# Kernel optimization log

Hardware: AMD Instinct MI355X
Metric: run time of the kernel (lower is better)

The kernel has to match this reference:

```python
import jax, jax.numpy as jnp
import numpy as np

B, L, D = 4, 2048, 1024
H, DK, DV, CS = 4, 128, 256, 16  # heads, head_qk_dim, head_v_dim, chunk_size
KD, VD = H * DK, H * DV          # 512, 1024
CONV = 4
EPS = 1e-5


def silu(x):
    return x * jax.nn.sigmoid(x)


def setup_inputs():
    key = jax.random.key(0)
    ks = jax.random.split(key, 9)
    s = 0.02
    return {
        "hidden_states": jax.random.normal(ks[0], (B, L, D), jnp.float32),
        "conv_w": jax.random.normal(ks[1], (D, CONV), jnp.float32) * 0.2,
        "Wq": jax.random.normal(ks[2], (KD, D), jnp.float32) * s,
        "Wk": jax.random.normal(ks[3], (KD, D), jnp.float32) * s,
        "Wv": jax.random.normal(ks[4], (VD, D), jnp.float32) * s,
        "Wb": jax.random.normal(ks[5], (H, D), jnp.float32) * s,
        "Wg": jax.random.normal(ks[6], (VD, D), jnp.float32) * s,
        "Wo": jax.random.normal(ks[7], (D, VD), jnp.float32) * s,
        "norm_w": jnp.ones((DV,), jnp.float32),
    }


def short_conv(x, w):
    # causal depthwise conv1d with SiLU activation: x [B,L,D], w [D,K]
    K = w.shape[1]
    xp = jnp.pad(x, ((0, 0), (K - 1, 0), (0, 0)))
    y = sum(xp[:, j:j + x.shape[1], :] * w[:, j] for j in range(K))
    return silu(y)


def delta_rule_chunk(q, k, v, beta):
    # fused_chunk_delta_rule: q,k [B,H,L,DK], v [B,H,L,DV], beta [B,H,L]
    b, h, l, dk = q.shape
    dv = v.shape[-1]
    nc = l // CS
    k = k * jax.lax.rsqrt(jnp.sum(k * k, -1, keepdims=True) + 1e-12)  # L2-normalize keys
    q = q * (dk ** -0.5)
    qc = q.reshape(b, h, nc, CS, dk)
    kc = k.reshape(b, h, nc, CS, dk)
    vc = v.reshape(b, h, nc, CS, dv)
    bc = beta.reshape(b, h, nc, CS)
    kb = kc * bc[..., None]
    # WY representation: T = (I + strict_tril(diag(beta) K K^T))^{-1}
    A = jnp.einsum('bhncd,bhnmd->bhncm', kb, kc)
    strict = jnp.tril(jnp.ones((CS, CS), q.dtype), -1)
    M = jnp.eye(CS, dtype=q.dtype) + A * strict
    eye = jnp.broadcast_to(jnp.eye(CS, dtype=q.dtype), M.shape)
    T = jax.scipy.linalg.solve_triangular(M, eye, lower=True)
    w = jnp.einsum('bhncm,bhnmd->bhncd', T, kb)
    u = jnp.einsum('bhncm,bhnmd->bhncd', T, vc * bc[..., None])
    causal = jnp.tril(jnp.ones((CS, CS), q.dtype))

    def step(S, inp):
        qi, ki, wi, ui = inp  # [B,H,CS,dk/dv]
        u_adj = ui - jnp.einsum('bhcd,bhdv->bhcv', wi, S)
        attn = jnp.einsum('bhcd,bhmd->bhcm', qi, ki) * causal
        o = jnp.einsum('bhcd,bhdv->bhcv', qi, S) + jnp.einsum('bhcm,bhmv->bhcv', attn, u_adj)
        S = S + jnp.einsum('bhcd,bhcv->bhdv', ki, u_adj)
        return S, o

    xs = tuple(jnp.moveaxis(t, 2, 0) for t in (qc, kc, w, u))
    S0 = jnp.zeros((b, h, dk, dv), q.dtype)
    _, os_ = jax.lax.scan(step, S0, xs)
    return jnp.moveaxis(os_, 0, 2).reshape(b, h, l, dv)


def reference(hidden_states, conv_w, Wq, Wk, Wv, Wb, Wg, Wo, norm_w):
    x = short_conv(hidden_states, conv_w)
    q = (x @ Wq.T).reshape(B, L, H, DK).transpose(0, 2, 1, 3)
    k = (x @ Wk.T).reshape(B, L, H, DK).transpose(0, 2, 1, 3)
    v = (x @ Wv.T).reshape(B, L, H, DV).transpose(0, 2, 1, 3)
    beta = jax.nn.sigmoid(x @ Wb.T).transpose(0, 2, 1)  # [B,H,L]
    o = delta_rule_chunk(q, k, v, beta)                 # [B,H,L,DV]
    o = o.transpose(0, 2, 1, 3)                          # [B,L,H,DV]
    g = (x @ Wg.T).reshape(B, L, H, DV)
    o = o * jax.lax.rsqrt(jnp.mean(o * o, -1, keepdims=True) + EPS) * norm_w * silu(g)
    return o.reshape(B, L, VD) @ Wo.T
```

## Files before the change

### kernel.cpp

```cpp
#include <hip/hip_runtime.h>
#include <cstdint>
#include <cstddef>

typedef _Float16 f16;
typedef _Float16 f16x4 __attribute__((ext_vector_type(4)));
typedef _Float16 f16x8 __attribute__((ext_vector_type(8)));
typedef float floatx4 __attribute__((ext_vector_type(4)));

#define MFMA32(a,b,c) __builtin_amdgcn_mfma_f32_16x16x32_f16((a),(b),(c),0,0,0)

#define ROWS 8192
#define NCHUNK 128
static constexpr float QSCALE = 0.08838834764831845f;

static __device__ __forceinline__ float sigmoidf_(float x) { return 1.0f / (1.0f + expf(-x)); }

static __device__ __forceinline__ uint32_t pack2(f16 a, f16 b) {
  union { f16 h[2]; uint32_t u; } v; v.h[0] = a; v.h[1] = b; return v.u;
}

#define GLOAD_LDS(gptr, lptr)                                                  \
  __builtin_amdgcn_global_load_lds(                                            \
      (const __attribute__((address_space(1))) void*)(gptr),                   \
      (__attribute__((address_space(3))) void*)(lptr), 16, 0, 0)

#define WAITV(N) do { asm volatile("s_waitcnt vmcnt(" #N ")" ::: "memory");    \
                      __builtin_amdgcn_sched_barrier(0); } while (0)

__global__ __launch_bounds__(256) void wconv_kernel(
    const float* __restrict__ Wq, const float* __restrict__ Wk,
    const float* __restrict__ Wv, const float* __restrict__ Wg,
    const float* __restrict__ Wo,
    f16* __restrict__ WcatHi, f16* __restrict__ WcatLoKV, f16* __restrict__ WoHi) {
  int tid = blockIdx.x * 256 + threadIdx.x;
  int e8 = tid * 8;
  if (e8 < 3145728) {
    int row = e8 >> 10, col = e8 & 1023;
    const float* src;
    if (row < 512)       src = Wk + (size_t)row * 1024 + col;
    else if (row < 1536) src = Wv + (size_t)(row - 512) * 1024 + col;
    else if (row < 2048) src = Wq + (size_t)(row - 1536) * 1024 + col;
    else                 src = Wg + (size_t)(row - 2048) * 1024 + col;
    f16 thi[8] __attribute__((aligned(16)));
    f16 tlo[8] __attribute__((aligned(16)));
#pragma unroll
    for (int j = 0; j < 8; j++) {
      float x = src[j];
      f16 h = (f16)x;
      thi[j] = h;
      tlo[j] = (f16)(x - (float)h);
    }
    *(uint4*)&WcatHi[e8] = *(const uint4*)thi;
    if (row < 1536) *(uint4*)&WcatLoKV[e8] = *(const uint4*)tlo;
  } else {
    int idx = e8 - 3145728;
    f16 t[8] __attribute__((aligned(16)));
#pragma unroll
    for (int j = 0; j < 8; j++) t[j] = (f16)Wo[idx + j];
    *(uint4*)&WoHi[idx] = *(const uint4*)t;
  }
}

__global__ __launch_bounds__(256) void conv_kernel(
    const float* __restrict__ hs, const float* __restrict__ cw,
    f16* __restrict__ xhi, f16* __restrict__ xlo) {
  int row = blockIdx.x;
  int b = row >> 11, l = row & 2047;
  int d = threadIdx.x * 4;
  floatx4 w0 = *(const floatx4*)&cw[(d + 0) * 4];
  floatx4 w1 = *(const floatx4*)&cw[(d + 1) * 4];
  floatx4 w2 = *(const floatx4*)&cw[(d + 2) * 4];
  floatx4 w3 = *(const floatx4*)&cw[(d + 3) * 4];
  floatx4 acc = {0.f, 0.f, 0.f, 0.f};
#pragma unroll
  for (int j = 0; j < 4; j++) {
    int ls = l - 3 + j;
    if (ls < 0) continue;
    floatx4 hv = *(const floatx4*)&hs[(size_t)(b * 2048 + ls) * 1024 + d];
    acc[0] += hv[0] * w0[j];
    acc[1] += hv[1] * w1[j];
    acc[2] += hv[2] * w2[j];
    acc[3] += hv[3] * w3[j];
  }
  f16 ohi[4] __attribute__((aligned(8)));
  f16 olo[4] __attribute__((aligned(8)));
#pragma unroll
  for (int q = 0; q < 4; q++) {
    float y = acc[q] * sigmoidf_(acc[q]);
    f16 h = (f16)y;
    ohi[q] = h;
    olo[q] = (f16)(y - (float)h);
  }
  *(uint2*)&xhi[(size_t)row * 1024 + d] = *(const uint2*)ohi;
  *(uint2*)&xlo[(size_t)row * 1024 + d] = *(const uint2*)olo;
}

__global__ __launch_bounds__(256) void beta_kernel(
    const f16* __restrict__ xhi, const f16* __restrict__ xlo,
    const float* __restrict__ Wb, float* __restrict__ betaf) {
  int row = blockIdx.x;
  int t = threadIdx.x;
  __shared__ floatx4 red[256];
  int c = t * 4;
  float xv[4];
#pragma unroll
  for (int j = 0; j < 4; j++)
    xv[j] = (float)xhi[(size_t)row * 1024 + c + j] + (float)xlo[(size_t)row * 1024 + c + j];
  floatx4 p = {0.f, 0.f, 0.f, 0.f};
#pragma unroll
  for (int hh = 0; hh < 4; hh++) {
    const float* wr = Wb + hh * 1024 + c;
    p[hh] = xv[0] * wr[0] + xv[1] * wr[1] + xv[2] * wr[2] + xv[3] * wr[3];
  }
  red[t] = p;
  __syncthreads();
  for (int s = 128; s > 0; s >>= 1) {
    if (t < s) red[t] += red[t + s];
    __syncthreads();
  }
  if (t < 4) betaf[(size_t)row * 4 + t] = sigmoidf_(red[0][t]);
}

__global__ __launch_bounds__(256) void gemm_hilo_kv(
    const f16* __restrict__ Ahi, const f16* __restrict__ Alo,
    const f16* __restrict__ Bhi, const f16* __restrict__ Blo,
    f16* __restrict__ ChHi, f16* __restrict__ ChLo, int K) {
  __shared__ __attribute__((aligned(16))) f16 AsH[128][40];
  __shared__ __attribute__((aligned(16))) f16 AsL[128][40];
  __shared__ __attribute__((aligned(16))) f16 BsH[128][40];
  __shared__ __attribute__((aligned(16))) f16 BsL[128][40];
  const int t = threadIdx.x;
  const int lane = t & 63, wave = t >> 6;
  const int lc = lane & 15, quad = lane >> 4;
  const int wm = (wave >> 1) * 64, wn = (wave & 1) * 64;
  const int m0 = blockIdx.y * 128, n0 = blockIdx.x * 128;
  const int r = t >> 2, c8 = (t & 3) * 8;
  floatx4 acc[4][4] = {};
  for (int kt = 0; kt < K; kt += 32) {
    __syncthreads();
    *(uint4*)&AsH[r][c8]      = *(const uint4*)&Ahi[(size_t)(m0 + r) * K + kt + c8];
    *(uint4*)&AsH[r + 64][c8] = *(const uint4*)&Ahi[(size_t)(m0 + r + 64) * K + kt + c8];
    *(uint4*)&AsL[r][c8]      = *(const uint4*)&Alo[(size_t)(m0 + r) * K + kt + c8];
    *(uint4*)&AsL[r + 64][c8] = *(const uint4*)&Alo[(size_t)(m0 + r + 64) * K + kt + c8];
    *(uint4*)&BsH[r][c8]      = *(const uint4*)&Bhi[(size_t)(n0 + r) * K + kt + c8];
    *(uint4*)&BsH[r + 64][c8] = *(const uint4*)&Bhi[(size_t)(n0 + r + 64) * K + kt + c8];
    *(uint4*)&BsL[r][c8]      = *(const uint4*)&Blo[(size_t)(n0 + r) * K + kt + c8];
    *(uint4*)&BsL[r + 64][c8] = *(const uint4*)&Blo[(size_t)(n0 + r + 64) * K + kt + c8];
    __syncthreads();
    f16x8 ah[4], al[4], bh2[4], bl[4];
#pragma unroll
    for (int i = 0; i < 4; i++) {
      ah[i] = *(const f16x8*)&AsH[wm + i * 16 + lc][quad * 8];
      al[i] = *(const f16x8*)&AsL[wm + i * 16 + lc][quad * 8];
    }
#pragma unroll
    for (int j = 0; j < 4; j++) {
      bh2[j] = *(const f16x8*)&BsH[wn + j * 16 + lc][quad * 8];
      bl[j]  = *(const f16x8*)&BsL[wn + j * 16 + lc][quad * 8];
    }
#pragma unroll
    for (int i = 0; i < 4; i++)
#pragma unroll
      for (int j = 0; j < 4; j++) {
        acc[i][j] = MFMA32(ah[i], bh2[j], acc[i][j]);
        acc[i][j] = MFMA32(al[i], bh2[j], acc[i][j]);
        acc[i][j] = MFMA32(ah[i], bl[j], acc[i][j]);
      }
  }
#pragma unroll
  for (int i = 0; i < 4; i++)
#pragma unroll
    for (int j = 0; j < 4; j++)
#pragma unroll
      for (int rr = 0; rr < 4; rr++) {
        int row = m0 + wm + i * 16 + quad * 4 + rr;
        int col = n0 + wn + j * 16 + lc;
        float x = acc[i][j][rr];
        f16 h = (f16)x;
        ChHi[(size_t)row * 3072 + col] = h;
        ChLo[(size_t)row * 1536 + col] = (f16)(x - (float)h);
      }
}

template <int OUTF16>
__global__ __launch_bounds__(256) void gemm_plain(
    const f16* __restrict__ A, const f16* __restrict__ Bw,
    f16* __restrict__ Ch, float* __restrict__ Cf, int K, int ldc) {
  __shared__ __attribute__((aligned(16))) f16 As[128][40];
  __shared__ __attribute__((aligned(16))) f16 Bs[128][40];
  const int t = threadIdx.x;
  const int lane = t & 63, wave = t >> 6;
  const int lc = lane & 15, quad = lane >> 4;
  const int wm = (wave >> 1) * 64, wn = (wave & 1) * 64;
  const int m0 = blockIdx.y * 128, n0 = blockIdx.x * 128;
  const int r = t >> 2, c8 = (t & 3) * 8;
  floatx4 acc[4][4] = {};
  for (int kt = 0; kt < K; kt += 32) {
    __syncthreads();
    *(uint4*)&As[r][c8]      = *(const uint4*)&A[(size_t)(m0 + r) * K + kt + c8];
    *(uint4*)&As[r + 64][c8] = *(const uint4*)&A[(size_t)(m0 + r + 64) * K + kt + c8];
    *(uint4*)&Bs[r][c8]      = *(const uint4*)&Bw[(size_t)(n0 + r) * K + kt + c8];
    *(uint4*)&Bs[r + 64][c8] = *(const uint4*)&Bw[(size_t)(n0 + r + 64) * K + kt + c8];
    __syncthreads();
    f16x8 af[4], bf[4];
#pragma unroll
    for (int i = 0; i < 4; i++) af[i] = *(const f16x8*)&As[wm + i * 16 + lc][quad * 8];
#pragma unroll
    for (int j = 0; j < 4; j++) bf[j] = *(const f16x8*)&Bs[wn + j * 16 + lc][quad * 8];
#pragma unroll
    for (int i = 0; i < 4; i++)
#pragma unroll
      for (int j = 0; j < 4; j++) acc[i][j] = MFMA32(af[i], bf[j], acc[i][j]);
  }
#pragma unroll
  for (int i = 0; i < 4; i++)
#pragma unroll
    for (int j = 0; j < 4; j++)
#pragma unroll
      for (int rr = 0; rr < 4; rr++) {
        int row = m0 + wm + i * 16 + quad * 4 + rr;
        int col = n0 + wn + j * 16 + lc;
        if (OUTF16) Ch[(size_t)row * ldc + col] = (f16)acc[i][j][rr];
        else        Cf[(size_t)row * ldc + col] = acc[i][j][rr];
      }
}

__global__ __launch_bounds__(256) void prepass_kernel(
    const f16* __restrict__ qkvgHi, const f16* __restrict__ kvLo,
    const float* __restrict__ betaf,
    f16* __restrict__ wHi, f16* __restrict__ wLo,
    f16* __restrict__ kTHi, f16* __restrict__ kTLo,
    f16* __restrict__ uHi, f16* __restrict__ uLo,
    float* __restrict__ attno) {
  int bid = blockIdx.x;
  int bh = bid >> 7, n = bid & 127;
  int b = bh >> 2, h = bh & 3;
  int t = threadIdx.x;

  __shared__ __attribute__((aligned(16))) float kc[16][132];
  __shared__ __attribute__((aligned(16))) float qc[16][132];
  __shared__ __attribute__((aligned(16))) float vb[16][260];
  __shared__ float Mm[16][16];
  __shared__ float Tt[16][16];
  __shared__ float Tb[16][16];
  __shared__ float part[16][16];
  __shared__ float betas[16];
  __shared__ float nrm[16];

  const size_t rowbase = (size_t)(b * 2048 + n * 16);
  {
    int i = t >> 4, o8 = (t & 15) * 8;
    size_t oh = (rowbase + i) * 3072;
    size_t ol = (rowbase + i) * 1536;
#pragma unroll
    for (int j = 0; j < 8; j++)
      kc[i][o8 + j] = (float)qkvgHi[oh + h * 128 + o8 + j] +
                      (float)kvLo[ol + h * 128 + o8 + j];
#pragma unroll
    for (int j = 0; j < 8; j++)
      qc[i][o8 + j] = (float)qkvgHi[oh + 1536 + h * 128 + o8 + j];
  }
  if (t < 16) betas[t] = betaf[(rowbase + t) * 4 + h];
  __syncthreads();
  {
    int i = t >> 4, sg = t & 15;
    float s = 0.f;
#pragma unroll
    for (int j = 0; j < 8; j++) { float v = kc[i][sg * 8 + j]; s += v * v; }
    part[i][sg] = s;
  }
  __syncthreads();
  if (t < 16) {
    float s = 0.f;
#pragma unroll
    for (int j = 0; j < 16; j++) s += part[t][j];
    nrm[t] = rsqrtf(s + 1e-12f);
  }
  __syncthreads();
  {
    int i = t >> 4, o8 = (t & 15) * 8;
    float sc = nrm[i];
#pragma unroll
    for (int j = 0; j < 8; j++) kc[i][o8 + j] *= sc;
  }
  __syncthreads();
  {
    int d = t & 127, ih = t >> 7;
    f16 thi[8] __attribute__((aligned(16)));
    f16 tlo[8] __attribute__((aligned(16)));
#pragma unroll
    for (int j = 0; j < 8; j++) {
      float x = kc[ih * 8 + j][d];
      f16 hh = (f16)x;
      thi[j] = hh;
      tlo[j] = (f16)(x - (float)hh);
    }
    size_t base = ((size_t)bh * 128 + n) * 2048 + d * 16 + ih * 8;
    *(uint4*)&kTHi[base] = *(const uint4*)thi;
    *(uint4*)&kTLo[base] = *(const uint4*)tlo;
  }
  {
    int i = t >> 4, j = t & 15;
    float s = 0.f;
    for (int x = 0; x < 128; x += 4)
      s += kc[i][x] * kc[j][x] + kc[i][x + 1] * kc[j][x + 1] +
           kc[i][x + 2] * kc[j][x + 2] + kc[i][x + 3] * kc[j][x + 3];
    Mm[i][j] = (i == j ? 1.f : 0.f) + ((j < i) ? betas[i] * s : 0.f);
  }
  __syncthreads();
  if (t < 16) {
    int j = t;
    float Tc[16];
#pragma unroll
    for (int i = 0; i < 16; i++) Tc[i] = 0.f;
    Tc[j] = 1.f;
    for (int i = j + 1; i < 16; i++) {
      float s = 0.f;
      for (int k2 = j; k2 < i; k2++) s += Mm[i][k2] * Tc[k2];
      Tc[i] = -s;
    }
    for (int i = 0; i < 16; i++) Tt[i][j] = Tc[i];
  }
  __syncthreads();
  { int i = t >> 4, m = t & 15; Tb[i][m] = Tt[i][m] * betas[m]; }
  {
    int m = t >> 4, c16 = (t & 15) * 16;
    size_t oh = (rowbase + m) * 3072 + 512 + h * 256 + c16;
    size_t ol = (rowbase + m) * 1536 + 512 + h * 256 + c16;
    float bm = betas[m];
#pragma unroll
    for (int j = 0; j < 16; j++)
      vb[m][c16 + j] = bm * ((float)qkvgHi[oh + j] + (float)kvLo[ol + j]);
  }
  __syncthreads();
  {
    int i = t >> 4, dg = t & 15;
    f16 thi[8] __attribute__((aligned(16)));
    f16 tlo[8] __attribute__((aligned(16)));
#pragma unroll
    for (int dd = 0; dd < 8; dd++) {
      int d = dg * 8 + dd;
      float s = 0.f;
#pragma unroll
      for (int m = 0; m < 16; m++) s += Tb[i][m] * kc[m][d];
      s = -s;
      f16 hh = (f16)s;
      thi[dd] = hh;
      tlo[dd] = (f16)(s - (float)hh);
    }
    size_t base = ((size_t)bh * 128 + n) * 2048 + i * 128 + dg * 8;
    *(uint4*)&wHi[base] = *(const uint4*)thi;
    *(uint4*)&wLo[base] = *(const uint4*)tlo;
  }
  {
    int v = t;
    f16 thi[16] __attribute__((aligned(16)));
    f16 tlo[16] __attribute__((aligned(16)));
#pragma unroll
    for (int i = 0; i < 16; i++) {
      float s2 = 0.f;
#pragma unroll
      for (int m = 0; m < 16; m++) s2 += Tt[i][m] * vb[m][v];
      f16 hh = (f16)s2;
      thi[i] = hh;
      tlo[i] = (f16)(s2 - (float)hh);
    }
    size_t base = ((((size_t)(v >> 4) * 16 + bh) * 128 + n) * 16 + (v & 15)) * 16;
    ((uint4*)&uHi[base])[0] = ((const uint4*)thi)[0];
    ((uint4*)&uHi[base])[1] = ((const uint4*)thi)[1];
    ((uint4*)&uLo[base])[0] = ((const uint4*)tlo)[0];
    ((uint4*)&uLo[base])[1] = ((const uint4*)tlo)[1];
  }
  {
    int i = t >> 4, j = t & 15;
    float s = 0.f;
    for (int x = 0; x < 128; x++) s += qc[i][x] * kc[j][x];
    attno[((size_t)bh * 128 + n) * 256 + i * 16 + j] = (j <= i) ? QSCALE * s : 0.f;
  }
}

#define STG_W   0
#define STG_WL  2048
#define STG_Q   4096
#define STG_KH  6144
#define STG_KL  8192
#define STG_SZ  10240

__global__ __launch_bounds__(64, 1) void scan_kernel(
    const f16* __restrict__ qkvgHi,
    const f16* __restrict__ wHi, const f16* __restrict__ wLo,
    const f16* __restrict__ kTHi, const f16* __restrict__ kTLo,
    const float* __restrict__ attn,
    const f16* __restrict__ uHi, const f16* __restrict__ uLo,
    float* __restrict__ o1, float* __restrict__ o2) {
  const int bid = blockIdx.x;
  const int slc = bid & 15, bh = bid >> 4;
  const int b = bh >> 2, h = bh & 3;
  const int v0 = slc * 16;
  const int lane = threadIdx.x;
  const int lc = lane & 15, quad = lane >> 4;
  const int qh = quad & 1;

  __shared__ __attribute__((aligned(16))) f16 stg[2][STG_SZ];
  __shared__ __attribute__((aligned(16))) f16 S_hi[16][136];
  __shared__ __attribute__((aligned(16))) f16 S_lo[16][136];

  floatx4 accS[8] = {};

  const size_t cb = (size_t)bh * 128;
  const f16* qb = qkvgHi + (size_t)b * 2048 * 3072 + 1536 + h * 128;
  const f16* ub  = uHi + ((size_t)(slc * 16 + bh)) * 0;
  (void)ub;
  const f16* ubH = uHi + ((size_t)(slc * 16 + bh)) * 128 * 256 + lc * 16 + quad * 4;
  const f16* ubL = uLo + ((size_t)(slc * 16 + bh)) * 128 * 256 + lc * 16 + quad * 4;
  const float* ab = attn + cb * 256 + lc * 16 + qh * 8;
  float* ob = (bh < 12) ? (o1 + (size_t)bh * 2048 * 256)
                        : (o2 + (size_t)(bh - 12) * 2048 * 256);

  int woff[4], koff[4], qoff[4];
#pragma unroll
  for (int p = 0; p < 4; p++) {
    int cid = p * 64 + lane;
    int row = cid >> 4, dgs = (cid & 15) ^ (row & 7);
    int d = cid >> 1,  ih = (cid & 1) ^ ((cid >> 3) & 1);
    woff[p] = row * 128 + dgs * 8;
    koff[p] = d * 16 + ih * 8;
    qoff[p] = row * 3072 + dgs * 8;
  }

  uint4 pa0[2], pa1[2];
  uint2 puh[2], pul[2];

  auto ISSUE_REG = [&](int slot, int nn) {
    pa0[slot] = *(const uint4*)(ab + (size_t)nn * 256);
    pa1[slot] = *(const uint4*)(ab + (size_t)nn * 256 + 4);
    puh[slot] = *(const uint2*)(ubH + (size_t)nn * 256);
    pul[slot] = *(const uint2*)(ubL + (size_t)nn * 256);
  };
  auto ISSUE_WQ = [&](int buf, int nn) {
    const f16* wsrc  = wHi + (cb + (size_t)nn) * 2048;
    const f16* wlsrc = wLo + (cb + (size_t)nn) * 2048;
    const f16* qsrc  = qb + (size_t)nn * 16 * 3072;
    f16* sbp = &stg[buf][0];
#pragma unroll
    for (int p = 0; p < 4; p++) {
      GLOAD_LDS(wsrc + woff[p],  sbp + STG_W  + p * 512);
      GLOAD_LDS(wlsrc + woff[p], sbp + STG_WL + p * 512);
      GLOAD_LDS(qsrc + qoff[p],  sbp + STG_Q  + p * 512);
    }
  };
  auto ISSUE_K = [&](int buf, int nn) {
    const f16* khsrc = kTHi + (cb + (size_t)nn) * 2048;
    const f16* klsrc = kTLo + (cb + (size_t)nn) * 2048;
    f16* sbp = &stg[buf][0];
#pragma unroll
    for (int p = 0; p < 4; p++) {
      GLOAD_LDS(khsrc + koff[p], sbp + STG_KH + p * 512);
      GLOAD_LDS(klsrc + koff[p], sbp + STG_KL + p * 512);
    }
  };

  ISSUE_REG(0, 0); ISSUE_WQ(0, 0); ISSUE_K(0, 0);
  ISSUE_REG(1, 1); ISSUE_WQ(1, 1); ISSUE_K(1, 1);

  for (int n = 0; n < NCHUNK; n += 2) {
#pragma unroll
    for (int hf = 0; hf < 2; hf++) {
      const int nn = n + hf;
      f16* sb = &stg[hf][0];

#pragma unroll
      for (int dt = 0; dt < 8; dt++) {
        f16x4 h4, l4;
#pragma unroll
        for (int r = 0; r < 4; r++) {
          float x = accS[dt][r];
          f16 hh = (f16)x;
          h4[r] = hh;
          l4[r] = (f16)(x - (float)hh);
        }
        *(f16x4*)&S_hi[lc][dt * 16 + quad * 4] = h4;
        *(f16x4*)&S_lo[lc][dt * 16 + quad * 4] = l4;
      }

      if (nn == 0)       WAITV(24);
      else if (nn < 127) WAITV(28);
      else               WAITV(4);

      floatx4 acc_u;
      {
        union { uint2 u2; f16 hh[4]; } Uh, Ul;
        Uh.u2 = puh[hf]; Ul.u2 = pul[hf];
#pragma unroll
        for (int r = 0; r < 4; r++) acc_u[r] = (float)Uh.hh[r] + (float)Ul.hh[r];
      }
      f16x8 aah, aal;
      {
        union { uint4 u4[2]; float f[8]; } PA;
        PA.u4[0] = pa0[hf]; PA.u4[1] = pa1[hf];
#pragma unroll
        for (int j = 0; j < 8; j++) {
          float a = PA.f[j];
          f16 ahh = (f16)a;
          aah[j] = ahh;
          aal[j] = (f16)(a - (float)ahh);
        }
      }
      if (nn + 2 < NCHUNK) ISSUE_REG(hf, nn + 2);

      f16x8 shf[4], slf[4], wah[4], wal[4], qah[4];
#pragma unroll
      for (int ks = 0; ks < 4; ks++) {
        shf[ks] = *(const f16x8*)&S_hi[lc][ks * 32 + quad * 8];
        slf[ks] = *(const f16x8*)&S_lo[lc][ks * 32 + quad * 8];
        int gi = lc * 128 + (((ks * 4 + quad) ^ (lc & 7)) * 8);
        wah[ks] = *(const f16x8*)(sb + STG_W  + gi);
        wal[ks] = *(const f16x8*)(sb + STG_WL + gi);
        qah[ks] = *(const f16x8*)(sb + STG_Q  + gi);
      }
      __builtin_amdgcn_sched_barrier(0);
      if (nn + 2 < NCHUNK) ISSUE_WQ(hf, nn + 2);

      floatx4 a1 = {0.f, 0.f, 0.f, 0.f}, a2 = {0.f, 0.f, 0.f, 0.f};
#pragma unroll
      for (int ks = 0; ks < 4; ks++) {
        acc_u = MFMA32(wah[ks], shf[ks], acc_u);
        a1    = MFMA32(wah[ks], slf[ks], a1);
        a2    = MFMA32(wal[ks], shf[ks], a2);
      }
      acc_u = acc_u + a1 + a2;
      floatx4 acc_o = {0.f, 0.f, 0.f, 0.f};
#pragma unroll
      for (int ks = 0; ks < 4; ks++) acc_o = MFMA32(qah[ks], shf[ks], acc_o);
#pragma unroll
      for (int ks = 0; ks < 4; ks++) acc_o = MFMA32(qah[ks], slf[ks], acc_o);

      f16x8 ubf;
      {
        f16 h0 = (f16)acc_u[0], h1 = (f16)acc_u[1];
        f16 h2 = (f16)acc_u[2], h3 = (f16)acc_u[3];
        uint32_t uh01 = pack2(h0, h1), uh23 = pack2(h2, h3);
        uint32_t ul01 = pack2((f16)(acc_u[0] - (float)h0), (f16)(acc_u[1] - (float)h1));
        uint32_t ul23 = pack2((f16)(acc_u[2] - (float)h2), (f16)(acc_u[3] - (float)h3));
        int srcA = (2 * qh) * 16 + lc;
        int srcB = srcA + 16;
        uint32_t Ah0 = __shfl((int)uh01, srcA, 64), Ah1 = __shfl((int)uh23, srcA, 64);
        uint32_t Bh0 = __shfl((int)uh01, srcB, 64), Bh1 = __shfl((int)uh23, srcB, 64);
        uint32_t Al0 = __shfl((int)ul01, srcA, 64), Al1 = __shfl((int)ul23, srcA, 64);
        uint32_t Bl0 = __shfl((int)ul01, srcB, 64), Bl1 = __shfl((int)ul23, srcB, 64);
        union { uint32_t u[4]; f16x8 v; } U;
        bool hi = (quad < 2);
        U.u[0] = hi ? Ah0 : Al0;
        U.u[1] = hi ? Ah1 : Al1;
        U.u[2] = hi ? Bh0 : Bl0;
        U.u[3] = hi ? Bh1 : Bl1;
        ubf = U.v;
      }
#pragma unroll
      for (int r = 0; r < 4; r++) acc_o[r] *= QSCALE;
      acc_o = MFMA32(aah, ubf, acc_o);
      acc_o = MFMA32(aal, ubf, acc_o);
#pragma unroll
      for (int r = 0; r < 4; r++)
        ob[(size_t)(nn * 16 + quad * 4 + r) * 256 + v0 + lc] = acc_o[r];

      const int kswz = (qh ^ ((lc >> 2) & 1)) * 8 + lc * 16;
#pragma unroll
      for (int dt = 0; dt < 8; dt++) {
        f16x8 kah = *(const f16x8*)(sb + STG_KH + dt * 256 + kswz);
        f16x8 kal = *(const f16x8*)(sb + STG_KL + dt * 256 + kswz);
        accS[dt] = MFMA32(kah, ubf, accS[dt]);
        accS[dt] = MFMA32(kal, ubf, accS[dt]);
      }
      __builtin_amdgcn_sched_barrier(0);
      if (nn + 2 < NCHUNK) ISSUE_K(hf, nn + 2);
    }
  }
}

__global__ __launch_bounds__(256) void gate_kernel(
    const float* __restrict__ o1, const float* __restrict__ o2,
    const f16* __restrict__ qkvgHi, const float* __restrict__ norm_w,
    f16* __restrict__ onh) {
  int h = threadIdx.x >> 6, lane = threadIdx.x & 63;
  int r = blockIdx.x;
  int b = r >> 11, l = r & 2047;
  int bh = b * 4 + h;
  const float* orow = ((bh < 12) ? (o1 + (size_t)bh * 524288)
                                 : (o2 + (size_t)(bh - 12) * 524288)) + (size_t)l * 256;
  int v = lane * 4;
  floatx4 ov = *(const floatx4*)&orow[v];
  float ss = ov[0] * ov[0] + ov[1] * ov[1] + ov[2] * ov[2] + ov[3] * ov[3];
  for (int m = 32; m > 0; m >>= 1) ss += __shfl_xor(ss, m);
  float rms = rsqrtf(ss * (1.0f / 256.0f) + 1e-5f);
  size_t goff = (size_t)r * 3072 + 2048 + h * 256 + v;
  floatx4 nw = *(const floatx4*)&norm_w[v];
  f16 outv[4] __attribute__((aligned(8)));
#pragma unroll
  for (int q2 = 0; q2 < 4; q2++) {
    float g = (float)qkvgHi[goff + q2];
    outv[q2] = (f16)(ov[q2] * rms * nw[q2] * (g * sigmoidf_(g)));
  }
  *(uint2*)&onh[(size_t)r * 1024 + h * 256 + v] = *(const uint2*)outv;
}

extern "C" void kernel_launch(void* const* d_in, const int* in_sizes, int n_in,
                              void* d_out, int out_size, void* d_ws, size_t ws_size,
                              hipStream_t stream) {
  (void)in_sizes; (void)n_in; (void)out_size; (void)ws_size;
  const float* hs     = (const float*)d_in[0];
  const float* conv_w = (const float*)d_in[1];
  const float* Wq     = (const float*)d_in[2];
  const float* Wk     = (const float*)d_in[3];
  const float* Wv     = (const float*)d_in[4];
  const float* Wb     = (const float*)d_in[5];
  const float* Wg     = (const float*)d_in[6];
  const float* Wo     = (const float*)d_in[7];
  const float* norm_w = (const float*)d_in[8];
  float* out = (float*)d_out;

  char* ws = (char*)d_ws;
  f16*   x_hi    = (f16*)(ws + 0);
  f16*   x_lo    = (f16*)(ws + 16777216);
  f16*   uHi     = (f16*)(ws + 0);
  f16*   uLo     = (f16*)(ws + 16777216);
  f16*   WcatHi  = (f16*)(ws + 33554432);
  float* o2f     = (float*)(ws + 33554432);
  f16*   WcatLo  = (f16*)(ws + 39845888);
  f16*   WoHi    = (f16*)(ws + 42991616);
  float* betaf   = (float*)(ws + 45088768);
  f16*   qkvgHi  = (f16*)(ws + 45219840);
  f16*   kvLo    = (f16*)(ws + 95551488);
  float* o1f     = (float*)(ws + 95551488);
  f16*   wHi     = (f16*)(ws + 120717312);
  f16*   on_h    = (f16*)(ws + 120717312);
  f16*   wLo     = (f16*)(ws + 129105920);
  f16*   kTHi    = (f16*)(ws + 137494528);
  f16*   kTLo    = (f16*)(ws + 145883136);
  float* attnf   = (float*)(ws + 154271744);

  wconv_kernel<<<2048, 256, 0, stream>>>(Wq, Wk, Wv, Wg, Wo, WcatHi, WcatLo, WoHi);
  conv_kernel<<<ROWS, 256, 0, stream>>>(hs, conv_w, x_hi, x_lo);
  beta_kernel<<<ROWS, 256, 0, stream>>>(x_hi, x_lo, Wb, betaf);
  gemm_hilo_kv<<<dim3(12, 64), 256, 0, stream>>>(
      x_hi, x_lo, WcatHi, WcatLo, qkvgHi, kvLo, 1024);
  gemm_plain<1><<<dim3(12, 64), 256, 0, stream>>>(
      x_hi, WcatHi + (size_t)1536 * 1024, qkvgHi + 1536, nullptr, 1024, 3072);
  prepass_kernel<<<16 * NCHUNK, 256, 0, stream>>>(
      qkvgHi, kvLo, betaf, wHi, wLo, kTHi, kTLo, uHi, uLo, attnf);
  scan_kernel<<<256, 64, 0, stream>>>(
      qkvgHi, wHi, wLo, kTHi, kTLo, attnf, uHi, uLo, o1f, o2f);
  gate_kernel<<<ROWS, 256, 0, stream>>>(o1f, o2f, qkvgHi, norm_w, on_h);
  gemm_plain<0><<<dim3(8, 64), 256, 0, stream>>>(
      on_h, WoHi, nullptr, out, 1024, 1024);
}
```

Baseline: 572.2 us.

## Use direct global-to-LDS loads with swizzle in GEMMs and reorder recurrence output work

Both projection GEMMs now stage tiles with global_load_lds into XOR-swizzled, unpadded shared buffers instead of loading through registers and storing to padded arrays. This removes the register round trip and the LDS padding while aiming to keep bank conflicts low on the MFMA fragment reads. In the delta-rule recurrence kernel, the output computation (q·S plus the intra-chunk attention term) moves after the state update and the K prefetch issue, and the vmcnt wait counts are raised to match. That lets the next K loads go out earlier, so the output MFMAs run while those loads are in flight.

```diff
diff --git a/kernel.cpp b/kernel.cpp
--- a/kernel.cpp
+++ b/kernel.cpp
@@ -26,6 +26,8 @@
 
 #define WAITV(N) do { asm volatile("s_waitcnt vmcnt(" #N ")" ::: "memory");    \
                       __builtin_amdgcn_sched_barrier(0); } while (0)
+
+#define SBAR() __builtin_amdgcn_sched_barrier(0)
 
 __global__ __launch_bounds__(256) void wconv_kernel(
     const float* __restrict__ Wq, const float* __restrict__ Wk,
@@ -125,38 +127,42 @@
     const f16* __restrict__ Ahi, const f16* __restrict__ Alo,
     const f16* __restrict__ Bhi, const f16* __restrict__ Blo,
     f16* __restrict__ ChHi, f16* __restrict__ ChLo, int K) {
-  __shared__ __attribute__((aligned(16))) f16 AsH[128][40];
-  __shared__ __attribute__((aligned(16))) f16 AsL[128][40];
-  __shared__ __attribute__((aligned(16))) f16 BsH[128][40];
-  __shared__ __attribute__((aligned(16))) f16 BsL[128][40];
+  __shared__ __attribute__((aligned(16))) f16 AsH[4096];
+  __shared__ __attribute__((aligned(16))) f16 AsL[4096];
+  __shared__ __attribute__((aligned(16))) f16 BsH[4096];
+  __shared__ __attribute__((aligned(16))) f16 BsL[4096];
   const int t = threadIdx.x;
   const int lane = t & 63, wave = t >> 6;
   const int lc = lane & 15, quad = lane >> 4;
   const int wm = (wave >> 1) * 64, wn = (wave & 1) * 64;
   const int m0 = blockIdx.y * 128, n0 = blockIdx.x * 128;
-  const int r = t >> 2, c8 = (t & 3) * 8;
+  const int scol = ((lane & 3) ^ ((lane >> 3) & 3)) * 8;
+  int srow[2];
+#pragma unroll
+  for (int pp = 0; pp < 2; pp++) srow[pp] = (wave * 2 + pp) * 16 + (lane >> 2);
+  const int swz = (quad ^ ((lc >> 1) & 3)) * 8;
   floatx4 acc[4][4] = {};
   for (int kt = 0; kt < K; kt += 32) {
     __syncthreads();
-    *(uint4*)&AsH[r][c8]      = *(const uint4*)&Ahi[(size_t)(m0 + r) * K + kt + c8];
-    *(uint4*)&AsH[r + 64][c8] = *(const uint4*)&Ahi[(size_t)(m0 + r + 64) * K + kt + c8];
-    *(uint4*)&AsL[r][c8]      = *(const uint4*)&Alo[(size_t)(m0 + r) * K + kt + c8];
-    *(uint4*)&AsL[r + 64][c8] = *(const uint4*)&Alo[(size_t)(m0 + r + 64) * K + kt + c8];
-    *(uint4*)&BsH[r][c8]      = *(const uint4*)&Bhi[(size_t)(n0 + r) * K + kt + c8];
-    *(uint4*)&BsH[r + 64][c8] = *(const uint4*)&Bhi[(size_t)(n0 + r + 64) * K + kt + c8];
-    *(uint4*)&BsL[r][c8]      = *(const uint4*)&Blo[(size_t)(n0 + r) * K + kt + c8];
-    *(uint4*)&BsL[r + 64][c8] = *(const uint4*)&Blo[(size_t)(n0 + r + 64) * K + kt + c8];
+#pragma unroll
+    for (int pp = 0; pp < 2; pp++) {
+      int ldso = (wave * 2 + pp) * 512;
+      GLOAD_LDS(&Ahi[(size_t)(m0 + srow[pp]) * K + kt + scol], AsH + ldso);
+      GLOAD_LDS(&Alo[(size_t)(m0 + srow[pp]) * K + kt + scol], AsL + ldso);
+      GLOAD_LDS(&Bhi[(size_t)(n0 + srow[pp]) * K + kt + scol], BsH + ldso);
+      GLOAD_LDS(&Blo[(size_t)(n0 + srow[pp]) * K + kt + scol], BsL + ldso);
+    }
     __syncthreads();
     f16x8 ah[4], al[4], bh2[4], bl[4];
 #pragma unroll
     for (int i = 0; i < 4; i++) {
-      ah[i] = *(const f16x8*)&AsH[wm + i * 16 + lc][quad * 8];
-      al[i] = *(const f16x8*)&AsL[wm + i * 16 + lc][quad * 8];
+      ah[i] = *(const f16x8*)&AsH[(wm + i * 16 + lc) * 32 + swz];
+      al[i] = *(const f16x8*)&AsL[(wm + i * 16 + lc) * 32 + swz];
     }
 #pragma unroll
     for (int j = 0; j < 4; j++) {
-      bh2[j] = *(const f16x8*)&BsH[wn + j * 16 + lc][quad * 8];
-      bl[j]  = *(const f16x8*)&BsL[wn + j * 16 + lc][quad * 8];
+      bh2[j] = *(const f16x8*)&BsH[(wn + j * 16 + lc) * 32 + swz];
+      bl[j]  = *(const f16x8*)&BsL[(wn + j * 16 + lc) * 32 + swz];
     }
 #pragma unroll
     for (int i = 0; i < 4; i++)
@@ -186,27 +192,33 @@
 __global__ __launch_bounds__(256) void gemm_plain(
     const f16* __restrict__ A, const f16* __restrict__ Bw,
     f16* __restrict__ Ch, float* __restrict__ Cf, int K, int ldc) {
-  __shared__ __attribute__((aligned(16))) f16 As[128][40];
-  __shared__ __attribute__((aligned(16))) f16 Bs[128][40];
+  __shared__ __attribute__((aligned(16))) f16 As[4096];
+  __shared__ __attribute__((aligned(16))) f16 Bs[4096];
   const int t = threadIdx.x;
   const int lane = t & 63, wave = t >> 6;
   const int lc = lane & 15, quad = lane >> 4;
   const int wm = (wave >> 1) * 64, wn = (wave & 1) * 64;
   const int m0 = blockIdx.y * 128, n0 = blockIdx.x * 128;
-  const int r = t >> 2, c8 = (t & 3) * 8;
+  const int scol = ((lane & 3) ^ ((lane >> 3) & 3)) * 8;
+  int srow[2];
+#pragma unroll
+  for (int pp = 0; pp < 2; pp++) srow[pp] = (wave * 2 + pp) * 16 + (lane >> 2);
+  const int swz = (quad ^ ((lc >> 1) & 3)) * 8;
   floatx4 acc[4][4] = {};
   for (int kt = 0; kt < K; kt += 32) {
     __syncthreads();
-    *(uint4*)&As[r][c8]      = *(const uint4*)&A[(size_t)(m0 + r) * K + kt + c8];
-    *(uint4*)&As[r + 64][c8] = *(const uint4*)&A[(size_t)(m0 + r + 64) * K + kt + c8];
-    *(uint4*)&Bs[r][c8]      = *(const uint4*)&Bw[(size_t)(n0 + r) * K + kt + c8];
-    *(uint4*)&Bs[r + 64][c8] = *(const uint4*)&Bw[(size_t)(n0 + r + 64) * K + kt + c8];
+#pragma unroll
+    for (int pp = 0; pp < 2; pp++) {
+      int ldso = (wave * 2 + pp) * 512;
+      GLOAD_LDS(&A[(size_t)(m0 + srow[pp]) * K + kt + scol],  As + ldso);
+      GLOAD_LDS(&Bw[(size_t)(n0 + srow[pp]) * K + kt + scol], Bs + ldso);
+    }
     __syncthreads();
     f16x8 af[4], bf[4];
 #pragma unroll
-    for (int i = 0; i < 4; i++) af[i] = *(const f16x8*)&As[wm + i * 16 + lc][quad * 8];
-#pragma unroll
-    for (int j = 0; j < 4; j++) bf[j] = *(const f16x8*)&Bs[wn + j * 16 + lc][quad * 8];
+    for (int i = 0; i < 4; i++) af[i] = *(const f16x8*)&As[(wm + i * 16 + lc) * 32 + swz];
+#pragma unroll
+    for (int j = 0; j < 4; j++) bf[j] = *(const f16x8*)&Bs[(wn + j * 16 + lc) * 32 + swz];
 #pragma unroll
     for (int i = 0; i < 4; i++)
 #pragma unroll
@@ -409,8 +421,6 @@
 
   const size_t cb = (size_t)bh * 128;
   const f16* qb = qkvgHi + (size_t)b * 2048 * 3072 + 1536 + h * 128;
-  const f16* ub  = uHi + ((size_t)(slc * 16 + bh)) * 0;
-  (void)ub;
   const f16* ubH = uHi + ((size_t)(slc * 16 + bh)) * 128 * 256 + lc * 16 + quad * 4;
   const f16* ubL = uLo + ((size_t)(slc * 16 + bh)) * 128 * 256 + lc * 16 + quad * 4;
   const float* ab = attn + cb * 256 + lc * 16 + qh * 8;
@@ -461,6 +471,7 @@
   };
 
   ISSUE_REG(0, 0); ISSUE_WQ(0, 0); ISSUE_K(0, 0);
+  SBAR();
   ISSUE_REG(1, 1); ISSUE_WQ(1, 1); ISSUE_K(1, 1);
 
   for (int n = 0; n < NCHUNK; n += 2) {
@@ -484,8 +495,9 @@
       }
 
       if (nn == 0)       WAITV(24);
-      else if (nn < 127) WAITV(28);
-      else               WAITV(4);
+      else if (nn == 1)  WAITV(28);
+      else if (nn < 127) WAITV(32);
+      else               WAITV(8);
 
       floatx4 acc_u;
       {
@@ -518,7 +530,7 @@
         wal[ks] = *(const f16x8*)(sb + STG_WL + gi);
         qah[ks] = *(const f16x8*)(sb + STG_Q  + gi);
       }
-      __builtin_amdgcn_sched_barrier(0);
+      SBAR();
       if (nn + 2 < NCHUNK) ISSUE_WQ(hf, nn + 2);
 
       floatx4 a1 = {0.f, 0.f, 0.f, 0.f}, a2 = {0.f, 0.f, 0.f, 0.f};
@@ -529,11 +541,6 @@
         a2    = MFMA32(wal[ks], shf[ks], a2);
       }
       acc_u = acc_u + a1 + a2;
-      floatx4 acc_o = {0.f, 0.f, 0.f, 0.f};
-#pragma unroll
-      for (int ks = 0; ks < 4; ks++) acc_o = MFMA32(qah[ks], shf[ks], acc_o);
-#pragma unroll
-      for (int ks = 0; ks < 4; ks++) acc_o = MFMA32(qah[ks], slf[ks], acc_o);
 
       f16x8 ubf;
       {
@@ -556,13 +563,6 @@
         U.u[3] = hi ? Bh1 : Bl1;
         ubf = U.v;
       }
-#pragma unroll
-      for (int r = 0; r < 4; r++) acc_o[r] *= QSCALE;
-      acc_o = MFMA32(aah, ubf, acc_o);
-      acc_o = MFMA32(aal, ubf, acc_o);
-#pragma unroll
-      for (int r = 0; r < 4; r++)
-        ob[(size_t)(nn * 16 + quad * 4 + r) * 256 + v0 + lc] = acc_o[r];
 
       const int kswz = (qh ^ ((lc >> 2) & 1)) * 8 + lc * 16;
 #pragma unroll
@@ -572,8 +572,22 @@
         accS[dt] = MFMA32(kah, ubf, accS[dt]);
         accS[dt] = MFMA32(kal, ubf, accS[dt]);
       }
-      __builtin_amdgcn_sched_barrier(0);
+      SBAR();
       if (nn + 2 < NCHUNK) ISSUE_K(hf, nn + 2);
+      SBAR();
+
+      floatx4 acc_o = {0.f, 0.f, 0.f, 0.f};
+#pragma unroll
+      for (int ks = 0; ks < 4; ks++) acc_o = MFMA32(qah[ks], shf[ks], acc_o);
+#pragma unroll
+      for (int ks = 0; ks < 4; ks++) acc_o = MFMA32(qah[ks], slf[ks], acc_o);
+#pragma unroll
+      for (int r = 0; r < 4; r++) acc_o[r] *= QSCALE;
+      acc_o = MFMA32(aah, ubf, acc_o);
+      acc_o = MFMA32(aal, ubf, acc_o);
+#pragma unroll
+      for (int r = 0; r < 4; r++)
+        ob[(size_t)(nn * 16 + quad * 4 + r) * 256 + v0 + lc] = acc_o[r];
     }
   }
 }
```

New measurement: 590.3 us. +3.2%, slower.
